# Performance work log

Hardware: AMD Instinct MI355X
Metric: run time of the kernel (lower is better)

The kernel has to match this reference:

```python
import jax, jax.numpy as jnp
import numpy as np

NUM_REGIONS = 29
OUT = 7          # RoIAlign output size
SR = 2           # sampling_ratio
IMG = 1024.0     # input image H = W
LN_EPS = 1e-5


def _layernorm(x, g, b):
    mu = jnp.mean(x, axis=-1, keepdims=True)
    var = jnp.mean(jnp.square(x - mu), axis=-1, keepdims=True)
    return (x - mu) * jax.lax.rsqrt(var + LN_EPS) * g + b


def _roi_align(fm, rois):
    """torchvision roi_align (aligned=False), spatial_scale=1.0, sampling_ratio=SR.
    fm: [B,C,H,W], rois: [B,R,4] (x1,y1,x2,y2 in feature coords). -> [B,R,C,OUT,OUT]"""
    B, C, H, W = fm.shape
    x1, y1, x2, y2 = jnp.moveaxis(rois, -1, 0)            # each [B,R]
    roi_w = jnp.maximum(x2 - x1, 1.0)
    roi_h = jnp.maximum(y2 - y1, 1.0)
    bw = roi_w / OUT
    bh = roi_h / OUT
    # sub-bin offsets: (bin + (s+0.5)/SR) for bin in [0,OUT), s in [0,SR)
    off = jnp.arange(OUT, dtype=jnp.float32)[:, None] + (jnp.arange(SR, dtype=jnp.float32)[None, :] + 0.5) / SR  # [OUT,SR]
    py = y1[..., None, None] + off * bh[..., None, None]  # [B,R,OUT,SR]
    px = x1[..., None, None] + off * bw[..., None, None]  # [B,R,OUT,SR]
    y = py[:, :, :, :, None, None]                        # [B,R,OUT,SR,1,1]
    x = px[:, :, None, None, :, :]                        # [B,R,1,1,OUT,SR]
    valid = (y >= -1.0) & (y <= H) & (x >= -1.0) & (x <= W)
    yc = jnp.clip(y, 0.0, H - 1.0)
    xc = jnp.clip(x, 0.0, W - 1.0)
    y0 = jnp.floor(yc).astype(jnp.int32)
    x0 = jnp.floor(xc).astype(jnp.int32)
    y1i = jnp.minimum(y0 + 1, H - 1)
    x1i = jnp.minimum(x0 + 1, W - 1)
    ly = yc - y0
    lx = xc - x0
    hy = 1.0 - ly
    hx = 1.0 - lx
    gather = jax.vmap(lambda f, yy, xx: f[:, yy, xx])     # per image: [C,H,W] -> [C,...]
    v00 = gather(fm, y0, x0)                              # [B,C,R,OUT,SR,OUT,SR]
    v01 = gather(fm, y0, x1i)
    v10 = gather(fm, y1i, x0)
    v11 = gather(fm, y1i, x1i)
    w00 = (hy * hx)[:, None]
    w01 = (hy * lx)[:, None]
    w10 = (ly * hx)[:, None]
    w11 = (ly * lx)[:, None]
    val = w00 * v00 + w01 * v01 + w10 * v10 + w11 * v11
    val = jnp.where(valid[:, None], val, 0.0)
    pooled = val.mean(axis=(4, 6))                        # average over SRxSR samples -> [B,C,R,OUT,OUT]
    return jnp.transpose(pooled, (0, 2, 1, 3, 4))         # [B,R,C,OUT,OUT]


def setup_inputs() -> dict:
    key = jax.random.key(0)
    ks = jax.random.split(key, 8)
    B, N, C, Hf, Wf, FD = 32, 40, 256, 64, 64, 768
    D = C * OUT * OUT
    feature_maps = jax.random.normal(ks[0], (B, C, Hf, Wf), jnp.float32)
    xy = jax.random.uniform(ks[1], (B, N, 2), jnp.float32) * 900.0
    wh = jax.random.uniform(ks[2], (B, N, 2), jnp.float32) * 100.0 + 16.0
    boxes = jnp.concatenate([xy, xy + wh], axis=-1)       # valid x1,y1,x2,y2 in image coords
    scores = jax.random.uniform(ks[3], (B, N), jnp.float32)
    labels = jax.random.randint(ks[4], (B, N), 0, NUM_REGIONS + 1)
    return {
        'feature_maps': feature_maps,
        'boxes': boxes,
        'scores': scores,
        'labels': labels,
        'w1': jax.random.normal(ks[5], (D, 2048), jnp.float32) * 0.02,
        'b1': jnp.zeros((2048,), jnp.float32),
        'g1': jnp.ones((2048,), jnp.float32),
        'be1': jnp.zeros((2048,), jnp.float32),
        'w2': jax.random.normal(ks[6], (2048, FD), jnp.float32) * 0.02,
        'b2': jnp.zeros((FD,), jnp.float32),
        'g2': jnp.ones((FD,), jnp.float32),
        'be2': jnp.zeros((FD,), jnp.float32),
        'missing_token': jax.random.normal(ks[7], (FD,), jnp.float32),
    }


def reference(feature_maps, boxes, scores, labels, w1, b1, g1, be1, w2, b2, g2, be2, missing_token):
    B, C, Hf, Wf = feature_maps.shape
    R = NUM_REGIONS
    scale = jnp.minimum(Hf / IMG, Wf / IMG)               # scale_factors (same for all images)
    # segmented argmax: best-scoring box per (image, region)
    region_idx = jnp.clip(labels, 1, R) - 1               # [B,N]
    onehot = region_idx[..., None] == jnp.arange(R)       # [B,N,R]
    masked = jnp.where(onehot, scores[..., None], -1.0)   # init best score = -1.0
    detected = jnp.any(onehot, axis=1)                    # [B,R]
    best = jnp.argmax(masked, axis=1)                     # [B,R] first max, matches strict-> loop
    sel = jnp.take_along_axis(boxes, jnp.broadcast_to(best[:, :, None], (B, R, 4)), axis=1)
    rois = sel * scale                                    # [B,R,4] in feature-map coords
    roi_feats = _roi_align(feature_maps, rois)            # [B,R,C,7,7]
    flat = roi_feats.reshape(B * R, C * OUT * OUT)
    h = _layernorm(flat @ w1 + b1, g1, be1)
    h = jax.nn.relu(h)
    h = _layernorm(h @ w2 + b2, g2, be2)                  # [B*R, feature_dim]
    feats = h.reshape(B, R, -1)
    region_features = jnp.where(detected[..., None], feats, missing_token)
    return region_features, detected
```

## Files before the change

kernel.cpp:

```cpp
#include <hip/hip_runtime.h>

typedef __bf16 bf16x8 __attribute__((ext_vector_type(8)));
typedef float f32x4 __attribute__((ext_vector_type(4)));
typedef unsigned short ushort8v __attribute__((ext_vector_type(8)));
typedef unsigned short ushort4v __attribute__((ext_vector_type(4)));

#define BATCH 32
#define NBOX 40
#define CCH 256
#define HF 64
#define WF 64
#define RREG 29
#define OUTP 7
#define MROWS 928
#define DDIM 12544
#define N1DIM 2048
#define FDIM 768
#define PDIM 4096
#define S1 8
#define S2 8

static constexpr size_t OFF_ROIS = 0;
static constexpr size_t OFF_DET  = 16384;
static constexpr size_t OFF_A    = 32768;
static constexpr size_t OFF_W1T  = OFF_A   + (size_t)MROWS * DDIM * 2;
static constexpr size_t OFF_FMT  = OFF_W1T;
static constexpr size_t OFF_W2T  = OFF_W1T + (size_t)DDIM * N1DIM * 2;
static constexpr size_t OFF_GP   = OFF_W2T + (size_t)N1DIM * FDIM * 2;
static constexpr size_t OFF_H    = OFF_W1T;

static __device__ __forceinline__ unsigned short f2bf(float f) {
  __bf16 h = (__bf16)f;
  return __builtin_bit_cast(unsigned short, h);
}
static __device__ __forceinline__ float bf2f(unsigned short u) {
  unsigned int x = ((unsigned int)u) << 16;
  return __builtin_bit_cast(float, x);
}
static __device__ __forceinline__ void gload_lds16(const void* g, void* l) {
  __builtin_amdgcn_global_load_lds((const __attribute__((address_space(1))) void*)g,
                                   (__attribute__((address_space(3))) void*)l, 16, 0, 0);
}

__global__ __launch_bounds__(256) void select_kernel(const float* __restrict__ boxes,
                                                     const float* __restrict__ scores,
                                                     const int* __restrict__ labels,
                                                     float* __restrict__ rois,
                                                     int* __restrict__ det,
                                                     float* __restrict__ out_det) {
  int tid = blockIdx.x * 256 + threadIdx.x;
  if (tid >= MROWS) return;
  int b = tid / RREG, r = tid % RREG;
  float bestS = -1.0f;
  int bestN = 0;
  int found = 0;
  for (int n = 0; n < NBOX; ++n) {
    int lab = labels[b * NBOX + n];
    int ri = min(max(lab, 1), RREG) - 1;
    if (ri == r) {
      found = 1;
      float s = scores[b * NBOX + n];
      if (s > bestS) { bestS = s; bestN = n; }
    }
  }
  const float scale = 0.0625f;
  float4 bx = *(const float4*)&boxes[(b * NBOX + bestN) * 4];
  rois[tid * 4 + 0] = bx.x * scale;
  rois[tid * 4 + 1] = bx.y * scale;
  rois[tid * 4 + 2] = bx.z * scale;
  rois[tid * 4 + 3] = bx.w * scale;
  det[tid] = found;
  out_det[tid] = found ? 1.0f : 0.0f;
}

__global__ __launch_bounds__(256) void fmt_kernel(const float* __restrict__ in,
                                                  unsigned short* __restrict__ out) {
  __shared__ float tile[64][65];
  int p0 = blockIdx.x * 64, c0 = blockIdx.y * 64, b = blockIdx.z;
  int t = threadIdx.x, tx = t & 15, ty = t >> 4;
#pragma unroll
  for (int q = 0; q < 4; ++q) {
    int r = ty + q * 16;
    float4 v = *(const float4*)&in[((long)b * CCH + c0 + r) * PDIM + p0 + tx * 4];
    tile[r][tx * 4 + 0] = v.x;
    tile[r][tx * 4 + 1] = v.y;
    tile[r][tx * 4 + 2] = v.z;
    tile[r][tx * 4 + 3] = v.w;
  }
  __syncthreads();
#pragma unroll
  for (int q = 0; q < 4; ++q) {
    int r = ty + q * 16;
    ushort4v o;
    o[0] = f2bf(tile[tx * 4 + 0][r]);
    o[1] = f2bf(tile[tx * 4 + 1][r]);
    o[2] = f2bf(tile[tx * 4 + 2][r]);
    o[3] = f2bf(tile[tx * 4 + 3][r]);
    *(ushort4v*)&out[((long)b * PDIM + p0 + r) * CCH + c0 + tx * 4] = o;
  }
}

__global__ __launch_bounds__(256) void roi_kernel(const unsigned short* __restrict__ fmT,
                                                  const float* __restrict__ rois,
                                                  unsigned short* __restrict__ A) {
  __shared__ int sidx[196][4];
  __shared__ float swt[196][4];
  __shared__ unsigned short Arow[DDIM];
  int roi = blockIdx.x;
  int t = threadIdx.x;
  float rx1 = rois[roi * 4 + 0], ry1 = rois[roi * 4 + 1];
  float rx2 = rois[roi * 4 + 2], ry2 = rois[roi * 4 + 3];
  float roiw = fmaxf(rx2 - rx1, 1.f), roih = fmaxf(ry2 - ry1, 1.f);
  float bw = roiw * (1.f / OUTP), bh = roih * (1.f / OUTP);
  if (t < 196) {
    int oy = t / 28, rem = t % 28, ox = rem / 4, s = rem % 4, sy = s >> 1, sx = s & 1;
    float y = ry1 + ((float)oy + ((float)sy + 0.5f) * 0.5f) * bh;
    float x = rx1 + ((float)ox + ((float)sx + 0.5f) * 0.5f) * bw;
    bool valid = (y >= -1.f) && (y <= 64.f) && (x >= -1.f) && (x <= 64.f);
    float yc = fminf(fmaxf(y, 0.f), 63.f);
    float xc = fminf(fmaxf(x, 0.f), 63.f);
    int y0 = (int)floorf(yc), x0 = (int)floorf(xc);
    int y1i = min(y0 + 1, 63), x1i = min(x0 + 1, 63);
    float ly = yc - (float)y0, lx = xc - (float)x0;
    float hy = 1.f - ly, hx = 1.f - lx;
    float m = valid ? 1.f : 0.f;
    swt[t][0] = hy * hx * m;
    swt[t][1] = hy * lx * m;
    swt[t][2] = ly * hx * m;
    swt[t][3] = ly * lx * m;
    sidx[t][0] = (y0 * 64 + x0) * CCH;
    sidx[t][1] = (y0 * 64 + x1i) * CCH;
    sidx[t][2] = (y1i * 64 + x0) * CCH;
    sidx[t][3] = (y1i * 64 + x1i) * CCH;
  }
  __syncthreads();
  int b = roi / RREG;
  int cg = t & 63;
  int sub = t >> 6;
  int start = sub * 12 + min(sub, 1);
  int cnt = sub == 0 ? 13 : 12;
  const unsigned short* base = fmT + (long)b * PDIM * CCH + cg * 4;
  for (int bi = 0; bi < cnt; ++bi) {
    int bin = start + bi;
    float a0 = 0.f, a1 = 0.f, a2 = 0.f, a3 = 0.f;
#pragma unroll
    for (int s = 0; s < 4; ++s) {
      int sid = bin * 4 + s;
#pragma unroll
      for (int tp = 0; tp < 4; ++tp) {
        float w = swt[sid][tp];
        ushort4v v = *(const ushort4v*)(base + sidx[sid][tp]);
        a0 += w * bf2f(v[0]);
        a1 += w * bf2f(v[1]);
        a2 += w * bf2f(v[2]);
        a3 += w * bf2f(v[3]);
      }
    }
    Arow[(cg * 4 + 0) * 49 + bin] = f2bf(a0 * 0.25f);
    Arow[(cg * 4 + 1) * 49 + bin] = f2bf(a1 * 0.25f);
    Arow[(cg * 4 + 2) * 49 + bin] = f2bf(a2 * 0.25f);
    Arow[(cg * 4 + 3) * 49 + bin] = f2bf(a3 * 0.25f);
  }
  __syncthreads();
  const ushort8v* src = (const ushort8v*)Arow;
  ushort8v* dst = (ushort8v*)(A + (long)roi * DDIM);
  for (int i = t; i < DDIM / 8; i += 256) dst[i] = src[i];
}

__global__ __launch_bounds__(256) void transpose_kernel(const float* __restrict__ in,
                                                        unsigned short* __restrict__ out,
                                                        int K, int N) {
  __shared__ float tile[64][65];
  int k0 = blockIdx.x * 64, n0 = blockIdx.y * 64;
  int t = threadIdx.x, tx = t & 15, ty = t >> 4;
#pragma unroll
  for (int p = 0; p < 4; ++p) {
    int r = ty + p * 16;
    float4 v = *(const float4*)&in[(long)(k0 + r) * N + n0 + tx * 4];
    tile[r][tx * 4 + 0] = v.x;
    tile[r][tx * 4 + 1] = v.y;
    tile[r][tx * 4 + 2] = v.z;
    tile[r][tx * 4 + 3] = v.w;
  }
  __syncthreads();
#pragma unroll
  for (int p = 0; p < 4; ++p) {
    int r = ty + p * 16;
    ushort4v o;
    o[0] = f2bf(tile[tx * 4 + 0][r]);
    o[1] = f2bf(tile[tx * 4 + 1][r]);
    o[2] = f2bf(tile[tx * 4 + 2][r]);
    o[3] = f2bf(tile[tx * 4 + 3][r]);
    *(ushort4v*)&out[(long)(n0 + r) * K + k0 + tx * 4] = o;
  }
}

__global__ __launch_bounds__(256, 3) void gemm_sk_kernel(const unsigned short* __restrict__ A,
                                                         const unsigned short* __restrict__ Bt,
                                                         float* __restrict__ Cp,
                                                         int M, int N, int K, int kchunk,
                                                         int gy, int q) {
  __shared__ unsigned short As[128 * 64];
  __shared__ unsigned short Bs[128 * 64];
  int bid = blockIdx.x;
  int tile = (bid & 7) * q + (bid >> 3);
  int bm = tile & 7;
  int rest = tile >> 3;
  int bn = rest % gy;
  int s = rest / gy;

  int t = threadIdx.x;
  int lane = t & 63, wv = t >> 6;
  int wr = wv >> 1, wc = wv & 1;
  int fr = lane & 15, fq = lane >> 4;

  f32x4 acc[4][4];
#pragma unroll
  for (int m = 0; m < 4; ++m)
#pragma unroll
    for (int n = 0; n < 4; ++n) acc[m][n] = (f32x4){0.f, 0.f, 0.f, 0.f};

  int srow = t >> 3;
  int scol = t & 7;
  int k_begin = s * kchunk;
  int k_end = min(k_begin + kchunk, K);

  int garow[4], gbrow[4], schunk[4];
#pragma unroll
  for (int i = 0; i < 4; ++i) {
    int row = srow + i * 32;
    schunk[i] = (scol ^ (row & 7)) * 8;
    garow[i] = min(bm * 128 + row, M - 1);
    gbrow[i] = bn * 128 + row;
  }

  for (int k0 = k_begin; k0 < k_end; k0 += 64) {
    __syncthreads();
#pragma unroll
    for (int i = 0; i < 4; ++i)
      gload_lds16(A + (long)garow[i] * K + k0 + schunk[i],
                  (char*)As + t * 16 + i * 4096);
#pragma unroll
    for (int i = 0; i < 4; ++i)
      gload_lds16(Bt + (long)gbrow[i] * K + k0 + schunk[i],
                  (char*)Bs + t * 16 + i * 4096);
    __syncthreads();

#pragma unroll
    for (int ks = 0; ks < 2; ++ks) {
      bf16x8 af[4], bfv[4];
#pragma unroll
      for (int m = 0; m < 4; ++m) {
        int row = wr * 64 + m * 16 + fr;
        int bc = (ks * 64 + fq * 16) ^ ((row & 7) << 4);
        af[m] = *(const bf16x8*)((const char*)As + row * 128 + bc);
      }
#pragma unroll
      for (int n = 0; n < 4; ++n) {
        int row = wc * 64 + n * 16 + fr;
        int bc = (ks * 64 + fq * 16) ^ ((row & 7) << 4);
        bfv[n] = *(const bf16x8*)((const char*)Bs + row * 128 + bc);
      }
#pragma unroll
      for (int m = 0; m < 4; ++m)
#pragma unroll
        for (int n = 0; n < 4; ++n)
          acc[m][n] = __builtin_amdgcn_mfma_f32_16x16x32_bf16(af[m], bfv[n], acc[m][n], 0, 0, 0);
    }
  }

  float* Cb = Cp + (long)s * M * N;
#pragma unroll
  for (int m = 0; m < 4; ++m)
#pragma unroll
    for (int n = 0; n < 4; ++n) {
      int col = bn * 128 + wc * 64 + n * 16 + fr;
#pragma unroll
      for (int j = 0; j < 4; ++j) {
        int row = bm * 128 + wr * 64 + m * 16 + fq * 4 + j;
        if (row < M) Cb[(long)row * N + col] = acc[m][n][j];
      }
    }
}

static __device__ __forceinline__ void block_reduce2(float& a, float& b, float* sm) {
#pragma unroll
  for (int off = 32; off > 0; off >>= 1) {
    a += __shfl_down(a, off);
    b += __shfl_down(b, off);
  }
  int lane = threadIdx.x & 63, wv = threadIdx.x >> 6;
  if (lane == 0) { sm[wv] = a; sm[wv + 4] = b; }
  __syncthreads();
  a = sm[0] + sm[1] + sm[2] + sm[3];
  b = sm[4] + sm[5] + sm[6] + sm[7];
}

__global__ __launch_bounds__(256) void ln1_kernel(const float* __restrict__ X,
                                                  const float* __restrict__ b1,
                                                  const float* __restrict__ g1,
                                                  const float* __restrict__ be1,
                                                  unsigned short* __restrict__ H) {
  __shared__ float sm[8];
  int row = blockIdx.x, t = threadIdx.x;
  float x[8];
  float sum = 0.f, sq = 0.f;
#pragma unroll
  for (int i = 0; i < 8; ++i) {
    int j = t + i * 256;
    float v = b1[j];
#pragma unroll
    for (int s = 0; s < S1; ++s) v += X[((long)s * MROWS + row) * N1DIM + j];
    x[i] = v;
    sum += v;
    sq += v * v;
  }
  block_reduce2(sum, sq, sm);
  float mu = sum * (1.f / N1DIM);
  float inv = rsqrtf(sq * (1.f / N1DIM) - mu * mu + 1e-5f);
#pragma unroll
  for (int i = 0; i < 8; ++i) {
    int j = t + i * 256;
    float y = fmaxf((x[i] - mu) * inv * g1[j] + be1[j], 0.f);
    H[(long)row * N1DIM + j] = f2bf(y);
  }
}

__global__ __launch_bounds__(256) void ln2_kernel(const float* __restrict__ X,
                                                  const float* __restrict__ b2,
                                                  const float* __restrict__ g2,
                                                  const float* __restrict__ be2,
                                                  const float* __restrict__ miss,
                                                  const int* __restrict__ det,
                                                  float* __restrict__ out) {
  __shared__ float sm[8];
  int row = blockIdx.x, t = threadIdx.x;
  float x[3];
  float sum = 0.f, sq = 0.f;
#pragma unroll
  for (int i = 0; i < 3; ++i) {
    int j = t + i * 256;
    float v = b2[j];
#pragma unroll
    for (int s = 0; s < S2; ++s) v += X[((long)s * MROWS + row) * FDIM + j];
    x[i] = v;
    sum += v;
    sq += v * v;
  }
  block_reduce2(sum, sq, sm);
  float mu = sum * (1.f / FDIM);
  float inv = rsqrtf(sq * (1.f / FDIM) - mu * mu + 1e-5f);
  int dv = det[row];
#pragma unroll
  for (int i = 0; i < 3; ++i) {
    int j = t + i * 256;
    float y = (x[i] - mu) * inv * g2[j] + be2[j];
    out[(long)row * FDIM + j] = dv ? y : miss[j];
  }
}

extern "C" void kernel_launch(void* const* d_in, const int* in_sizes, int n_in,
                              void* d_out, int out_size, void* d_ws, size_t ws_size,
                              hipStream_t stream) {
  const float* fm     = (const float*)d_in[0];
  const float* boxes  = (const float*)d_in[1];
  const float* scores = (const float*)d_in[2];
  const int*   labels = (const int*)d_in[3];
  const float* w1     = (const float*)d_in[4];
  const float* b1     = (const float*)d_in[5];
  const float* g1     = (const float*)d_in[6];
  const float* be1    = (const float*)d_in[7];
  const float* w2     = (const float*)d_in[8];
  const float* b2     = (const float*)d_in[9];
  const float* g2     = (const float*)d_in[10];
  const float* be2    = (const float*)d_in[11];
  const float* miss   = (const float*)d_in[12];
  float* out = (float*)d_out;
  char* ws = (char*)d_ws;

  float* rois = (float*)(ws + OFF_ROIS);
  int* det = (int*)(ws + OFF_DET);
  unsigned short* Abf = (unsigned short*)(ws + OFF_A);
  unsigned short* fmT = (unsigned short*)(ws + OFF_FMT);
  unsigned short* w1t = (unsigned short*)(ws + OFF_W1T);
  unsigned short* w2t = (unsigned short*)(ws + OFF_W2T);
  float* Gp = (float*)(ws + OFF_GP);
  unsigned short* Hbf = (unsigned short*)(ws + OFF_H);

  hipLaunchKernelGGL(select_kernel, dim3(4), dim3(256), 0, stream,
                     boxes, scores, labels, rois, det, out + (long)MROWS * FDIM);
  hipLaunchKernelGGL(fmt_kernel, dim3(PDIM / 64, CCH / 64, BATCH), dim3(256), 0, stream,
                     fm, fmT);
  hipLaunchKernelGGL(roi_kernel, dim3(MROWS), dim3(256), 0, stream, fmT, rois, Abf);
  hipLaunchKernelGGL(transpose_kernel, dim3(DDIM / 64, N1DIM / 64), dim3(256), 0, stream,
                     w1, w1t, DDIM, N1DIM);
  hipLaunchKernelGGL(transpose_kernel, dim3(N1DIM / 64, FDIM / 64), dim3(256), 0, stream,
                     w2, w2t, N1DIM, FDIM);
  {
    int nkb = DDIM / 64;
    int kc = ((nkb + S1 - 1) / S1) * 64;
    int gy = N1DIM / 128, nwg = 8 * gy * S1;
    hipLaunchKernelGGL(gemm_sk_kernel, dim3(nwg), dim3(256), 0, stream,
                       Abf, w1t, Gp, MROWS, N1DIM, DDIM, kc, gy, nwg / 8);
  }
  hipLaunchKernelGGL(ln1_kernel, dim3(MROWS), dim3(256), 0, stream, Gp, b1, g1, be1, Hbf);
  {
    int nkb = N1DIM / 64;
    int kc = ((nkb + S2 - 1) / S2) * 64;
    int gy = FDIM / 128, nwg = 8 * gy * S2;
    hipLaunchKernelGGL(gemm_sk_kernel, dim3(nwg), dim3(256), 0, stream,
                       Hbf, w2t, Gp, MROWS, FDIM, N1DIM, kc, gy, nwg / 8);
  }
  hipLaunchKernelGGL(ln2_kernel, dim3(MROWS), dim3(256), 0, stream,
                     Gp, b2, g2, be2, miss, det, out);
}
```

Baseline: 191.0 us.

## Double-buffer GEMM LDS loads and merge small launch kernels

The split-K GEMM now uses two LDS buffers and prefetches the next two K-tiles with async global-to-LDS loads. A partial vmcnt wait lets memory traffic overlap the MFMA work instead of the previous load, barrier, compute sequence. Doubling LDS lowers the occupancy hint from 3 to 2 blocks per CU. The select and feature-map format kernels are merged into one launch, as are the two weight transposes, to save launch overhead.

```diff
diff --git a/kernel.cpp b/kernel.cpp
--- a/kernel.cpp
+++ b/kernel.cpp
@@ -42,42 +42,45 @@
                                    (__attribute__((address_space(3))) void*)l, 16, 0, 0);
 }
 
-__global__ __launch_bounds__(256) void select_kernel(const float* __restrict__ boxes,
+__global__ __launch_bounds__(256) void selfmt_kernel(const float* __restrict__ in,
+                                                     unsigned short* __restrict__ out,
+                                                     const float* __restrict__ boxes,
                                                      const float* __restrict__ scores,
                                                      const int* __restrict__ labels,
                                                      float* __restrict__ rois,
                                                      int* __restrict__ det,
                                                      float* __restrict__ out_det) {
-  int tid = blockIdx.x * 256 + threadIdx.x;
-  if (tid >= MROWS) return;
-  int b = tid / RREG, r = tid % RREG;
-  float bestS = -1.0f;
-  int bestN = 0;
-  int found = 0;
-  for (int n = 0; n < NBOX; ++n) {
-    int lab = labels[b * NBOX + n];
-    int ri = min(max(lab, 1), RREG) - 1;
-    if (ri == r) {
-      found = 1;
-      float s = scores[b * NBOX + n];
-      if (s > bestS) { bestS = s; bestN = n; }
+  __shared__ float tile[64][65];
+  int bid = blockIdx.x;
+  int t = threadIdx.x;
+  if (bid >= PDIM / 64 * (CCH / 64) * BATCH) {
+    int tid = (bid - PDIM / 64 * (CCH / 64) * BATCH) * 256 + t;
+    if (tid >= MROWS) return;
+    int b = tid / RREG, r = tid % RREG;
+    float bestS = -1.0f;
+    int bestN = 0;
+    int found = 0;
+    for (int n = 0; n < NBOX; ++n) {
+      int lab = labels[b * NBOX + n];
+      int ri = min(max(lab, 1), RREG) - 1;
+      if (ri == r) {
+        found = 1;
+        float s = scores[b * NBOX + n];
+        if (s > bestS) { bestS = s; bestN = n; }
+      }
     }
-  }
-  const float scale = 0.0625f;
-  float4 bx = *(const float4*)&boxes[(b * NBOX + bestN) * 4];
-  rois[tid * 4 + 0] = bx.x * scale;
-  rois[tid * 4 + 1] = bx.y * scale;
-  rois[tid * 4 + 2] = bx.z * scale;
-  rois[tid * 4 + 3] = bx.w * scale;
-  det[tid] = found;
-  out_det[tid] = found ? 1.0f : 0.0f;
-}
-
-__global__ __launch_bounds__(256) void fmt_kernel(const float* __restrict__ in,
-                                                  unsigned short* __restrict__ out) {
-  __shared__ float tile[64][65];
-  int p0 = blockIdx.x * 64, c0 = blockIdx.y * 64, b = blockIdx.z;
-  int t = threadIdx.x, tx = t & 15, ty = t >> 4;
+    const float scale = 0.0625f;
+    float4 bx = *(const float4*)&boxes[(b * NBOX + bestN) * 4];
+    rois[tid * 4 + 0] = bx.x * scale;
+    rois[tid * 4 + 1] = bx.y * scale;
+    rois[tid * 4 + 2] = bx.z * scale;
+    rois[tid * 4 + 3] = bx.w * scale;
+    det[tid] = found;
+    out_det[tid] = found ? 1.0f : 0.0f;
+    return;
+  }
+  int p0 = (bid & 63) * 64, c0 = ((bid >> 6) & 3) * 64, b = bid >> 8;
+  int tx = t & 15, ty = t >> 4;
 #pragma unroll
   for (int q = 0; q < 4; ++q) {
     int r = ty + q * 16;
@@ -167,11 +170,25 @@
   for (int i = t; i < DDIM / 8; i += 256) dst[i] = src[i];
 }
 
-__global__ __launch_bounds__(256) void transpose_kernel(const float* __restrict__ in,
-                                                        unsigned short* __restrict__ out,
-                                                        int K, int N) {
+__global__ __launch_bounds__(256) void wT_kernel(const float* __restrict__ w1,
+                                                 unsigned short* __restrict__ w1t,
+                                                 const float* __restrict__ w2,
+                                                 unsigned short* __restrict__ w2t) {
   __shared__ float tile[64][65];
-  int k0 = blockIdx.x * 64, n0 = blockIdx.y * 64;
+  int bid = blockIdx.x;
+  const float* in;
+  unsigned short* out;
+  int K, N, k0, n0;
+  if (bid < (DDIM / 64) * (N1DIM / 64)) {
+    in = w1; out = w1t; K = DDIM; N = N1DIM;
+    k0 = (bid % (DDIM / 64)) * 64;
+    n0 = (bid / (DDIM / 64)) * 64;
+  } else {
+    int r = bid - (DDIM / 64) * (N1DIM / 64);
+    in = w2; out = w2t; K = N1DIM; N = FDIM;
+    k0 = (r % (N1DIM / 64)) * 64;
+    n0 = (r / (N1DIM / 64)) * 64;
+  }
   int t = threadIdx.x, tx = t & 15, ty = t >> 4;
 #pragma unroll
   for (int p = 0; p < 4; ++p) {
@@ -195,13 +212,13 @@
   }
 }
 
-__global__ __launch_bounds__(256, 3) void gemm_sk_kernel(const unsigned short* __restrict__ A,
+__global__ __launch_bounds__(256, 2) void gemm_sk_kernel(const unsigned short* __restrict__ A,
                                                          const unsigned short* __restrict__ Bt,
                                                          float* __restrict__ Cp,
                                                          int M, int N, int K, int kchunk,
                                                          int gy, int q) {
-  __shared__ unsigned short As[128 * 64];
-  __shared__ unsigned short Bs[128 * 64];
+  __shared__ unsigned short As[2 * 128 * 64];
+  __shared__ unsigned short Bs[2 * 128 * 64];
   int bid = blockIdx.x;
   int tile = (bid & 7) * q + (bid >> 3);
   int bm = tile & 7;
@@ -224,6 +241,7 @@
   int scol = t & 7;
   int k_begin = s * kchunk;
   int k_end = min(k_begin + kchunk, K);
+  int nkt = (k_end - k_begin) >> 6;
 
   int garow[4], gbrow[4], schunk[4];
 #pragma unroll
@@ -234,18 +252,30 @@
     gbrow[i] = bn * 128 + row;
   }
 
-  for (int k0 = k_begin; k0 < k_end; k0 += 64) {
-    __syncthreads();
-#pragma unroll
-    for (int i = 0; i < 4; ++i)
-      gload_lds16(A + (long)garow[i] * K + k0 + schunk[i],
-                  (char*)As + t * 16 + i * 4096);
-#pragma unroll
-    for (int i = 0; i < 4; ++i)
-      gload_lds16(Bt + (long)gbrow[i] * K + k0 + schunk[i],
-                  (char*)Bs + t * 16 + i * 4096);
-    __syncthreads();
-
+#define GSTAGE(buf, kt_) do {                                                  \
+    int k0_ = k_begin + (kt_) * 64;                                            \
+    _Pragma("unroll")                                                          \
+    for (int i = 0; i < 4; ++i)                                                \
+      gload_lds16(A + (long)garow[i] * K + k0_ + schunk[i],                    \
+                  (char*)As + (buf) * 16384 + t * 16 + i * 4096);              \
+    _Pragma("unroll")                                                          \
+    for (int i = 0; i < 4; ++i)                                                \
+      gload_lds16(Bt + (long)gbrow[i] * K + k0_ + schunk[i],                   \
+                  (char*)Bs + (buf) * 16384 + t * 16 + i * 4096);              \
+  } while (0)
+
+  GSTAGE(0, 0);
+  GSTAGE(1, min(1, nkt - 1));
+
+  for (int kt = 0; kt < nkt; ++kt) {
+    int cur = kt & 1;
+    asm volatile("s_waitcnt vmcnt(8)" ::: "memory");
+    __builtin_amdgcn_sched_barrier(0);
+    __builtin_amdgcn_s_barrier();
+    __builtin_amdgcn_sched_barrier(0);
+
+    const char* Ab = (const char*)As + cur * 16384;
+    const char* Bb = (const char*)Bs + cur * 16384;
 #pragma unroll
     for (int ks = 0; ks < 2; ++ks) {
       bf16x8 af[4], bfv[4];
@@ -253,13 +283,13 @@
       for (int m = 0; m < 4; ++m) {
         int row = wr * 64 + m * 16 + fr;
         int bc = (ks * 64 + fq * 16) ^ ((row & 7) << 4);
-        af[m] = *(const bf16x8*)((const char*)As + row * 128 + bc);
+        af[m] = *(const bf16x8*)(Ab + row * 128 + bc);
       }
 #pragma unroll
       for (int n = 0; n < 4; ++n) {
         int row = wc * 64 + n * 16 + fr;
         int bc = (ks * 64 + fq * 16) ^ ((row & 7) << 4);
-        bfv[n] = *(const bf16x8*)((const char*)Bs + row * 128 + bc);
+        bfv[n] = *(const bf16x8*)(Bb + row * 128 + bc);
       }
 #pragma unroll
       for (int m = 0; m < 4; ++m)
@@ -267,7 +297,13 @@
         for (int n = 0; n < 4; ++n)
           acc[m][n] = __builtin_amdgcn_mfma_f32_16x16x32_bf16(af[m], bfv[n], acc[m][n], 0, 0, 0);
     }
-  }
+
+    __builtin_amdgcn_sched_barrier(0);
+    __builtin_amdgcn_s_barrier();
+    __builtin_amdgcn_sched_barrier(0);
+    GSTAGE(cur, min(kt + 2, nkt - 1));
+  }
+#undef GSTAGE
 
   float* Cb = Cp + (long)s * M * N;
 #pragma unroll
@@ -387,15 +423,11 @@
   float* Gp = (float*)(ws + OFF_GP);
   unsigned short* Hbf = (unsigned short*)(ws + OFF_H);
 
-  hipLaunchKernelGGL(select_kernel, dim3(4), dim3(256), 0, stream,
-                     boxes, scores, labels, rois, det, out + (long)MROWS * FDIM);
-  hipLaunchKernelGGL(fmt_kernel, dim3(PDIM / 64, CCH / 64, BATCH), dim3(256), 0, stream,
-                     fm, fmT);
+  hipLaunchKernelGGL(selfmt_kernel, dim3(8192 + 4), dim3(256), 0, stream,
+                     fm, fmT, boxes, scores, labels, rois, det, out + (long)MROWS * FDIM);
   hipLaunchKernelGGL(roi_kernel, dim3(MROWS), dim3(256), 0, stream, fmT, rois, Abf);
-  hipLaunchKernelGGL(transpose_kernel, dim3(DDIM / 64, N1DIM / 64), dim3(256), 0, stream,
-                     w1, w1t, DDIM, N1DIM);
-  hipLaunchKernelGGL(transpose_kernel, dim3(N1DIM / 64, FDIM / 64), dim3(256), 0, stream,
-                     w2, w2t, N1DIM, FDIM);
+  hipLaunchKernelGGL(wT_kernel, dim3((DDIM / 64) * (N1DIM / 64) + (N1DIM / 64) * (FDIM / 64)),
+                     dim3(256), 0, stream, w1, w1t, w2, w2t);
   {
     int nkb = DDIM / 64;
     int kc = ((nkb + S1 - 1) / S1) * 64;
```

After: 190.0 us (median of 2 runs). No clear change (-0.5%).
